# Optimization experiments

Hardware: AMD Instinct MI355X
Metric: run time of the kernel (lower is better)

## Reference

```python
import jax, jax.numpy as jnp
import numpy as np

NV, D, C, S, H, W = 50, 32, 16, 64, 64, 64  # views, volume res, feat ch, samples/ray, ray grid


def _conv(x, w, b, stride):
    y = jax.lax.conv_general_dilated(x, w, (stride, stride), 'SAME',
                                     dimension_numbers=('NCHW', 'OIHW', 'NCHW'))
    return y + b[None, :, None, None]


def setup_inputs():
    key = jax.random.key(0)
    k = jax.random.split(key, 16)
    images = jax.random.normal(k[0], (NV, 3, 128, 128), jnp.float32)
    # target_rays channels: [origin(3), dir(3), near(1), far(1)]
    o = (jax.random.uniform(k[1], (1, 3, H, W), jnp.float32) - 0.5) * 0.2
    d = jax.random.normal(k[2], (1, 3, H, W), jnp.float32)
    d = d / jnp.linalg.norm(d, axis=1, keepdims=True)
    near = jnp.full((1, 1, H, W), 0.2, jnp.float32)
    far = jnp.full((1, 1, H, W), 1.2, jnp.float32)
    target_rays = jnp.concatenate([o, d, near, far], axis=1)
    s = 0.1
    return {
        'images': images, 'target_rays': target_rays,
        'w1': jax.random.normal(k[3], (64, 3, 3, 3), jnp.float32) * s, 'b1': jnp.zeros((64,), jnp.float32),
        'w2': jax.random.normal(k[4], (128, 64, 3, 3), jnp.float32) * s, 'b2': jnp.zeros((128,), jnp.float32),
        'w3': jax.random.normal(k[5], (C * D, 128, 3, 3), jnp.float32) * s, 'b3': jnp.zeros((C * D,), jnp.float32),
        'mw1': jax.random.normal(k[6], (C, 64), jnp.float32) * s, 'mb1': jnp.zeros((64,), jnp.float32),
        'mw2': jax.random.normal(k[7], (64, 64), jnp.float32) * s, 'mb2': jnp.zeros((64,), jnp.float32),
        'mw3': jax.random.normal(k[8], (64, 4), jnp.float32) * s, 'mb3': jnp.zeros((4,), jnp.float32),
    }


def _forward(images, target_rays, w1, b1, w2, b2, w3, b3, mw1, mb1, mw2, mb2, mw3, mb3):
    # FeatureVolumeEncoder: [NV,3,128,128] -> per-view volume [NV,C,D,D,D]
    x = jax.nn.relu(_conv(images, w1, b1, 2))   # [NV,64,64,64]
    x = jax.nn.relu(_conv(x, w2, b2, 2))        # [NV,128,32,32]
    x = _conv(x, w3, b3, 1)                     # [NV,C*D,32,32]
    volumes = x.reshape(NV, C, D, D, D)
    # mean over views first: gather indices are identical per view, so
    # mean(gather(vol_i)) == gather(mean(vol_i)) by linearity (original means after sampling)
    vol = volumes.mean(axis=0)                  # [C,D,D,D]

    # sample_coarse_points: stratified z samples along each ray
    o, dirs = target_rays[0, 0:3], target_rays[0, 3:6]   # [3,H,W]
    near, far = target_rays[0, 6], target_rays[0, 7]     # [H,W]
    t = jnp.linspace(0.0, 1.0, S).astype(target_rays.dtype)[:, None, None]
    z = near[None] + (far - near)[None] * t              # [S,H,W]
    pts = o[:, None] + dirs[:, None] * z[None]           # [3,S,H,W]
    pts = pts.transpose(1, 2, 3, 0).reshape(-1, 3)       # [N,3], N=S*H*W

    # sample_from_3dgrid: trilinear interpolation, pts in [-1,1]^3
    c = jnp.clip((pts + 1.0) * 0.5 * (D - 1), 0.0, D - 1.0)
    c0 = jnp.minimum(jnp.floor(c).astype(jnp.int32), D - 2)
    f = c - c0
    ix, iy, iz = c0[:, 0], c0[:, 1], c0[:, 2]
    fx, fy, fz = f[:, 0], f[:, 1], f[:, 2]
    def g(dz, dy, dx):
        return vol[:, iz + dz, iy + dy, ix + dx]  # [C,N] irregular gather
    feat = (g(0, 0, 0) * (1 - fz) * (1 - fy) * (1 - fx) + g(0, 0, 1) * (1 - fz) * (1 - fy) * fx
          + g(0, 1, 0) * (1 - fz) * fy * (1 - fx) + g(0, 1, 1) * (1 - fz) * fy * fx
          + g(1, 0, 0) * fz * (1 - fy) * (1 - fx) + g(1, 0, 1) * fz * (1 - fy) * fx
          + g(1, 1, 0) * fz * fy * (1 - fx) + g(1, 1, 1) * fz * fy * fx)  # [C,N]
    feat = feat.T  # [N,C]

    # MLP_Nerf: 16 -> 64 -> 64 -> 4 (rgb, sigma)
    h = jax.nn.relu(feat @ mw1 + mb1)
    h = jax.nn.relu(h @ mw2 + mb2)
    raw = (h @ mw3 + mb3).reshape(S, H, W, 4)
    rgb = jax.nn.sigmoid(raw[..., :3])   # [S,H,W,3]
    sigma = jax.nn.relu(raw[..., 3])     # [S,H,W]

    # composite: quadrature alpha-compositing along samples
    deltas = jnp.concatenate([z[1:] - z[:-1], jnp.full((1, H, W), 1e10, z.dtype)], axis=0)
    alpha = 1.0 - jnp.exp(-sigma * deltas)
    trans = jnp.cumprod(1.0 - alpha + 1e-10, axis=0)
    trans = jnp.concatenate([jnp.ones((1, H, W), z.dtype), trans[:-1]], axis=0)
    wts = alpha * trans                  # [S,H,W]
    rgb_final = jnp.einsum('shw,shwc->chw', wts, rgb)[None, None]   # [1,1,3,H,W]
    depth_final = jnp.sum(wts * z, axis=0)[None, None, None]        # [1,1,1,H,W]
    return rgb_final, depth_final


def reference(images, target_rays, w1, b1, w2, b2, w3, b3, mw1, mb1, mw2, mb2, mw3, mb3):
    return _forward(images, target_rays, w1, b1, w2, b2, w3, b3, mw1, mb1, mw2, mb2, mw3, mb3)
```

## Files before the change

kernel.cpp:

```cpp
#include <hip/hip_runtime.h>
#include <hip/hip_bf16.h>

#define NVV 50
#define C1 64
#define C2 128
#define HW1 64
#define HW2 32

typedef short bf16x8 __attribute__((ext_vector_type(8)));
typedef short s16x4 __attribute__((ext_vector_type(4)));
typedef float f32x4 __attribute__((ext_vector_type(4)));
typedef int i32x4 __attribute__((ext_vector_type(4)));

__device__ inline short f2bf(float x) {
    unsigned u = __builtin_bit_cast(unsigned, x);
    unsigned r = (u + 0x7FFFu + ((u >> 16) & 1u)) >> 16;
    return (short)r;
}
__device__ inline float bf2f(short x) {
    unsigned u = ((unsigned)(unsigned short)x) << 16;
    return __builtin_bit_cast(float, u);
}

__global__ __launch_bounds__(256) void pack_all(const float* __restrict__ w1,
                                                const float* __restrict__ w2,
                                                const float* __restrict__ w3,
                                                const float* __restrict__ mw1, const float* __restrict__ mb1,
                                                const float* __restrict__ mw2, const float* __restrict__ mw3,
                                                __hip_bfloat16* __restrict__ WPK1,
                                                __hip_bfloat16* __restrict__ WPK2,
                                                __hip_bfloat16* __restrict__ WPK3,
                                                __hip_bfloat16* __restrict__ WPM1,
                                                __hip_bfloat16* __restrict__ WPM2,
                                                __hip_bfloat16* __restrict__ WPM3) {
    int i = blockIdx.x * 256 + threadIdx.x;
    if (i < 2048) {
        int j = i & 7, l = (i >> 3) & 63, mf = i >> 9;
        int oc = mf * 16 + (l & 15);
        int k = (l >> 4) * 8 + j;
        WPK1[i] = __float2bfloat16(k < 27 ? w1[oc * 27 + k] : 0.f);
    } else if (i < 75776) {
        int q = i - 2048;
        int j = q & 7, l = (q >> 3) & 63;
        int rest = q >> 9;
        int mtile = rest & 7;
        rest >>= 3;
        int icb = rest & 1;
        int kk = rest >> 1;
        int oc = mtile * 16 + (l & 15);
        int ic = icb * 32 + (l >> 4) * 8 + j;
        int ky = kk / 3, kx = kk % 3;
        WPK2[q] = __float2bfloat16(w2[((oc * 64 + ic) * 3 + ky) * 3 + kx]);
    } else if (i < 665600) {
        int q = i - 75776;
        int j = q & 7, l = (q >> 3) & 63;
        int rest = q >> 9;
        int m = rest & 31;
        rest >>= 5;
        int icb = rest & 3;
        int kk = rest >> 2;
        int oc = m * 16 + (l & 15);
        int ic = icb * 32 + (l >> 4) * 8 + j;
        int ky = kk / 3, kx = kk % 3;
        WPK3[q] = __float2bfloat16(w3[((oc * 128 + ic) * 3 + ky) * 3 + kx]);
    } else if (i < 672768) {
        int q = i - 665600;
        if (q < 2048) {
            int j = q & 7, l = (q >> 3) & 63, mf = q >> 9;
            int nn = mf * 16 + (l & 15);
            int ch = (l >> 4) * 8 + j;
            float v = ch < 16 ? mw1[ch * 64 + nn] : (ch == 16 ? mb1[nn] : 0.f);
            WPM1[q] = __float2bfloat16(v);
        } else if (q < 6144) {
            int p = q - 2048;
            int j = p & 7, l = (p >> 3) & 63, f = p >> 9;
            int kb = f >> 2, mf = f & 3;
            int nn = mf * 16 + (l & 15);
            int k = kb * 32 + (l >> 4) * 8 + j;
            WPM2[p] = __float2bfloat16(mw2[k * 64 + nn]);
        } else {
            int p = q - 6144;
            int j = p & 7, l = (p >> 3) & 63, kb = p >> 9;
            int m = l & 15;
            int k = kb * 32 + (l >> 4) * 8 + j;
            WPM3[p] = __float2bfloat16(m < 4 ? mw3[k * 4 + m] : 0.f);
        }
    }
}


__global__ __launch_bounds__(256) void conv1_fused(const float* __restrict__ img,
                                                   const __hip_bfloat16* __restrict__ wpack,
                                                   const float* __restrict__ b1,
                                                   __hip_bfloat16* __restrict__ out) {
    __shared__ float tile[3 * 9 * 132];
    int b = blockIdx.x;
    int xcd = b & 7, slot = b >> 3;
    int v = xcd + 8 * (slot >> 4);
    int oyb = slot & 15;
    if (v >= NVV) return;
    int tid = threadIdx.x;
    const float* ip = img + (size_t)v * 3 * 128 * 128;
    int iy0 = oyb * 8;
    for (int idx = tid; idx < 3456; idx += 256) {
        int ix = idx & 127;
        int t = idx >> 7;
        int iyl = t % 9, ic = t / 9;
        int iy = iy0 + iyl;
        tile[(ic * 9 + iyl) * 132 + ix] = (iy < 128) ? ip[(ic * 128 + iy) * 128 + ix] : 0.f;
    }
    if (tid < 108) {
        int c = tid & 3;
        int t = tid >> 2;
        int iyl = t % 9, ic = t / 9;
        tile[(ic * 9 + iyl) * 132 + 128 + c] = 0.f;
    }
    __syncthreads();

    int l = tid & 63, w = tid >> 6;
    int lane16 = l & 15, lgrp = l >> 4;
    int oy = oyb * 4 + w;

    int offj[8];
    bool okj[8];
    #pragma unroll
    for (int j = 0; j < 8; ++j) {
        int k = lgrp * 8 + j;
        bool ok = k < 27;
        int kc = ok ? k : 0;
        int ic = kc / 9, r = kc % 9;
        int ky = r / 3, kx = r % 3;
        offj[j] = (ic * 9 + 2 * w + ky) * 132 + kx;
        okj[j] = ok;
    }

    bf16x8 a[4];
    #pragma unroll
    for (int mf = 0; mf < 4; ++mf)
        a[mf] = *(const bf16x8*)((const short*)wpack + (mf * 64 + l) * 8);

    f32x4 acc[4][4];
    #pragma unroll
    for (int mf = 0; mf < 4; ++mf)
        #pragma unroll
        for (int nf = 0; nf < 4; ++nf)
            acc[mf][nf] = (f32x4){0.f, 0.f, 0.f, 0.f};

    #pragma unroll
    for (int nf = 0; nf < 4; ++nf) {
        int ox = nf * 16 + lane16;
        bf16x8 bb;
        #pragma unroll
        for (int j = 0; j < 8; ++j) {
            float x = tile[offj[j] + 2 * ox];
            bb[j] = okj[j] ? f2bf(x) : (short)0;
        }
        #pragma unroll
        for (int mf = 0; mf < 4; ++mf)
            acc[mf][nf] = __builtin_amdgcn_mfma_f32_16x16x32_bf16(a[mf], bb, acc[mf][nf], 0, 0, 0);
    }

    #pragma unroll
    for (int mf = 0; mf < 4; ++mf) {
        #pragma unroll
        for (int nf = 0; nf < 4; ++nf) {
            int px = (v * 64 + oy) * 64 + nf * 16 + lane16;
            s16x4 sv;
            #pragma unroll
            for (int r = 0; r < 4; ++r) {
                int oc = mf * 16 + lgrp * 4 + r;
                sv[r] = f2bf(fmaxf(acc[mf][nf][r] + b1[oc], 0.f));
            }
            *(s16x4*)((short*)out + (size_t)px * 64 + mf * 16 + lgrp * 4) = sv;
        }
    }
}

__global__ __launch_bounds__(128) void conv2_mfma(const __hip_bfloat16* __restrict__ A1c,
                                                  const __hip_bfloat16* __restrict__ wpack,
                                                  const float* __restrict__ b2,
                                                  __hip_bfloat16* __restrict__ A2c) {
    int b = blockIdx.x;
    int xcd = b & 7, slot = b >> 3;
    int v = xcd + 8 * (slot >> 4);
    int oyb = slot & 15;
    if (v >= NVV) return;
    int tid = threadIdx.x;
    int l = tid & 63;
    int wm = tid >> 6;
    int lane16 = l & 15, lgrp = l >> 4;

    int oxv[4], oyv[4];
    const short* pxb[4];
    bool rOOB[4], cOOB[4];
    const short* ibase = (const short*)A1c + (size_t)v * 64 * 64 * 64;
    #pragma unroll
    for (int nf = 0; nf < 4; ++nf) {
        int px = nf * 16 + lane16;
        int dy = px >> 5, ox = px & 31;
        oxv[nf] = ox;
        oyv[nf] = oyb * 2 + dy;
        pxb[nf] = ibase + ((size_t)(2 * oyv[nf]) * 64 + 2 * ox) * 64 + lgrp * 8;
        rOOB[nf] = (oyv[nf] == 31);
        cOOB[nf] = (ox == 31);
    }

    f32x4 acc[4][4];
    #pragma unroll
    for (int mf = 0; mf < 4; ++mf)
        #pragma unroll
        for (int nf = 0; nf < 4; ++nf)
            acc[mf][nf] = (f32x4){0.f, 0.f, 0.f, 0.f};

    const short* ab = (const short*)wpack + wm * 4 * 512 + l * 8;
    const bf16x8 bz = (bf16x8){0, 0, 0, 0, 0, 0, 0, 0};

    #pragma unroll
    for (int kk = 0; kk < 9; ++kk) {
        const int ky = kk / 3, kx = kk % 3;
        #pragma unroll
        for (int icb = 0; icb < 2; ++icb) {
            bf16x8 a[4];
            #pragma unroll
            for (int mf = 0; mf < 4; ++mf)
                a[mf] = *(const bf16x8*)(ab + ((kk * 2 + icb) * 8 + mf) * 512);

            bf16x8 bb[4];
            #pragma unroll
            for (int nf = 0; nf < 4; ++nf) {
                bf16x8 t = *(const bf16x8*)(pxb[nf] + (ky * 64 + kx) * 64 + icb * 32);
                bool dead = (ky == 2 && rOOB[nf]) || (kx == 2 && cOOB[nf]);
                bb[nf] = dead ? bz : t;
            }
            #pragma unroll
            for (int mf = 0; mf < 4; ++mf)
                #pragma unroll
                for (int nf = 0; nf < 4; ++nf)
                    acc[mf][nf] = __builtin_amdgcn_mfma_f32_16x16x32_bf16(a[mf], bb[nf], acc[mf][nf], 0, 0, 0);
        }
    }

    #pragma unroll
    for (int nf = 0; nf < 4; ++nf) {
        int pix = oyv[nf] * 32 + oxv[nf];
        short* ob = (short*)A2c + ((size_t)v * 1024 + pix) * 128 + wm * 64;
        #pragma unroll
        for (int mf = 0; mf < 4; ++mf) {
            f32x4 bv = *(const f32x4*)(b2 + wm * 64 + mf * 16 + lgrp * 4);
            s16x4 sv;
            #pragma unroll
            for (int r = 0; r < 4; ++r) sv[r] = f2bf(fmaxf(acc[mf][nf][r] + bv[r], 0.f));
            *(s16x4*)(ob + mf * 16 + lgrp * 4) = sv;
        }
    }
}

__global__ __launch_bounds__(256) void mean_kernel(const __hip_bfloat16* __restrict__ A2c,
                                                   __hip_bfloat16* __restrict__ XBc) {
    int i = blockIdx.x * 256 + threadIdx.x;
    int g = i & 15, pix = i >> 4;
    float acc[8] = {0.f, 0.f, 0.f, 0.f, 0.f, 0.f, 0.f, 0.f};
    for (int v = 0; v < NVV; ++v) {
        bf16x8 x = *(const bf16x8*)((const short*)A2c + ((size_t)v * 1024 + pix) * 128 + g * 8);
        #pragma unroll
        for (int j = 0; j < 8; ++j) acc[j] += bf2f(x[j]);
    }
    bf16x8 o;
    #pragma unroll
    for (int j = 0; j < 8; ++j) o[j] = f2bf(acc[j] * (1.0f / NVV));
    *(bf16x8*)((short*)XBc + (size_t)pix * 128 + g * 8) = o;
}

__global__ __launch_bounds__(128) void conv3_mfma(const __hip_bfloat16* __restrict__ XBc,
                                                  const __hip_bfloat16* __restrict__ wpack,
                                                  const float* __restrict__ b3,
                                                  __hip_bfloat16* __restrict__ VOLc) {
    int tid = threadIdx.x;
    int l = tid & 63;
    int wn = tid >> 6;
    int lane16 = l & 15, lgrp = l >> 4;

    int px = blockIdx.y * 32 + wn * 16 + lane16;
    int y = px >> 5, x = px & 31;

    const short* pxb = (const short*)XBc + ((ptrdiff_t)(y - 1) * 32 + (x - 1)) * 128 + lgrp * 8;
    bool tOOB = (y == 0), bOOB = (y == 31), lOOB = (x == 0), rOOB = (x == 31);

    f32x4 acc[4];
    #pragma unroll
    for (int mf = 0; mf < 4; ++mf) acc[mf] = (f32x4){0.f, 0.f, 0.f, 0.f};

    const short* ab = (const short*)wpack + (size_t)blockIdx.x * 4 * 512 + l * 8;
    const bf16x8 bzv = (bf16x8){0, 0, 0, 0, 0, 0, 0, 0};

    #pragma unroll
    for (int kk = 0; kk < 9; ++kk) {
        const int ky = kk / 3, kx = kk % 3;
        bool dead = (ky == 0 && tOOB) || (ky == 2 && bOOB) || (kx == 0 && lOOB) || (kx == 2 && rOOB);
        #pragma unroll
        for (int icb = 0; icb < 4; ++icb) {
            bf16x8 t = *(const bf16x8*)(pxb + (ky * 32 + kx) * 128 + icb * 32);
            bf16x8 bb = dead ? bzv : t;
            #pragma unroll
            for (int mf = 0; mf < 4; ++mf) {
                bf16x8 a = *(const bf16x8*)(ab + (size_t)((kk * 4 + icb) * 32 + mf) * 512);
                acc[mf] = __builtin_amdgcn_mfma_f32_16x16x32_bf16(a, bb, acc[mf], 0, 0, 0);
            }
        }
    }

    int oc_base = blockIdx.x * 64;
    #pragma unroll
    for (int mf = 0; mf < 4; ++mf) {
        f32x4 bv = *(const f32x4*)(b3 + oc_base + mf * 16 + lgrp * 4);
        #pragma unroll
        for (int r = 0; r < 4; ++r) {
            int oc = oc_base + mf * 16 + lgrp * 4 + r;
            int c = oc >> 5, iz = oc & 31;
            VOLc[((size_t)((iz * 32 + y) * 32 + x)) * 16 + c] = __float2bfloat16(acc[mf][r] + bv[r]);
        }
    }
}

__global__ __launch_bounds__(256) void mlp_render(const __hip_bfloat16* __restrict__ VOLc,
                                                  const float* __restrict__ rays,
                                                  const __hip_bfloat16* __restrict__ wpm1,
                                                  const __hip_bfloat16* __restrict__ wpm2,
                                                  const __hip_bfloat16* __restrict__ wpm3,
                                                  const float* __restrict__ mb2,
                                                  const float* __restrict__ mb3,
                                                  float* __restrict__ out) {
    __shared__ short hbuf[4][32 * 72];
    __shared__ f32x4 rawb[4][64];
    int tid = threadIdx.x;
    int w = tid >> 6, l = tid & 63;
    int lane16 = l & 15, lgrp = l >> 4;
    short* hb = hbuf[w];
    int pix = blockIdx.x * 4 + w;

    bf16x8 a1[4];
    #pragma unroll
    for (int mf = 0; mf < 4; ++mf)
        a1[mf] = *(const bf16x8*)((const short*)wpm1 + (mf * 64 + l) * 8);
    bf16x8 a2[2][4];
    #pragma unroll
    for (int kb = 0; kb < 2; ++kb)
        #pragma unroll
        for (int mf = 0; mf < 4; ++mf)
            a2[kb][mf] = *(const bf16x8*)((const short*)wpm2 + ((kb * 4 + mf) * 64 + l) * 8);
    bf16x8 a3[2];
    a3[0] = *(const bf16x8*)((const short*)wpm3 + (0 * 64 + l) * 8);
    a3[1] = *(const bf16x8*)((const short*)wpm3 + (1 * 64 + l) * 8);
    f32x4 b3v = *(const f32x4*)(mb3);

    const bf16x8 bz = (bf16x8){0, 0, 0, 0, 0, 0, 0, 0};
    const bf16x8 bbias = (bf16x8){(short)0x3F80, 0, 0, 0, 0, 0, 0, 0};

    float o0 = rays[pix], o1 = rays[4096 + pix], o2 = rays[2 * 4096 + pix];
    float d0 = rays[3 * 4096 + pix], d1 = rays[4 * 4096 + pix], d2 = rays[5 * 4096 + pix];
    float nearv = rays[6 * 4096 + pix], farv = rays[7 * 4096 + pix];

    int nfg = l >> 5, hf = (l >> 4) & 1;

    for (int rep = 0; rep < 2; ++rep) {
        int s = rep * 32 + nfg * 16 + lane16;
        float t = (float)s / 63.0f;
        float z = nearv + (farv - nearv) * t;
        float px = o0 + d0 * z, py = o1 + d1 * z, pz = o2 + d2 * z;
        float cx = fminf(fmaxf((px + 1.f) * 15.5f, 0.f), 31.f);
        float cy = fminf(fmaxf((py + 1.f) * 15.5f, 0.f), 31.f);
        float cz = fminf(fmaxf((pz + 1.f) * 15.5f, 0.f), 31.f);
        int ix = min((int)floorf(cx), 30);
        int iy = min((int)floorf(cy), 30);
        int iz = min((int)floorf(cz), 30);
        float fx = cx - (float)ix, fy = cy - (float)iy, fz = cz - (float)iz;
        float gx = 1.f - fx, gy = 1.f - fy, gz = 1.f - fz;
        float wv[8] = {gz * gy * gx, gz * gy * fx, gz * fy * gx, gz * fy * fx,
                       fz * gy * gx, fz * gy * fx, fz * fy * gx, fz * fy * fx};
        const int co[8] = {0, 16, 512, 528, 16384, 16400, 16896, 16912};
        int base = (iz * 32 + iy) * 32 + ix;
        const short* vp = (const short*)VOLc + (size_t)base * 16 + hf * 8;

        float f8[8] = {0.f, 0.f, 0.f, 0.f, 0.f, 0.f, 0.f, 0.f};
        #pragma unroll
        for (int c = 0; c < 8; ++c) {
            bf16x8 cv = *(const bf16x8*)(vp + co[c]);
            #pragma unroll
            for (int j = 0; j < 8; ++j) f8[j] += wv[c] * bf2f(cv[j]);
        }
        bf16x8 own;
        #pragma unroll
        for (int j = 0; j < 8; ++j) own[j] = f2bf(f8[j]);

        i32x4 oi = __builtin_bit_cast(i32x4, own);
        i32x4 si;
        si[0] = __shfl_xor(oi[0], 32);
        si[1] = __shfl_xor(oi[1], 32);
        si[2] = __shfl_xor(oi[2], 32);
        si[3] = __shfl_xor(oi[3], 32);
        bf16x8 swf = __builtin_bit_cast(bf16x8, si);

        bf16x8 b0 = (lgrp < 2) ? own : ((lgrp == 2) ? bbias : bz);
        bf16x8 b1 = (lgrp < 2) ? swf : ((lgrp == 2) ? bbias : bz);

        f32x4 acc1[4][2];
        #pragma unroll
        for (int mf = 0; mf < 4; ++mf) {
            acc1[mf][0] = (f32x4){0.f, 0.f, 0.f, 0.f};
            acc1[mf][1] = (f32x4){0.f, 0.f, 0.f, 0.f};
            acc1[mf][0] = __builtin_amdgcn_mfma_f32_16x16x32_bf16(a1[mf], b0, acc1[mf][0], 0, 0, 0);
            acc1[mf][1] = __builtin_amdgcn_mfma_f32_16x16x32_bf16(a1[mf], b1, acc1[mf][1], 0, 0, 0);
        }
        #pragma unroll
        for (int mf = 0; mf < 4; ++mf) {
            #pragma unroll
            for (int nf = 0; nf < 2; ++nf) {
                s16x4 sv;
                #pragma unroll
                for (int r = 0; r < 4; ++r) sv[r] = f2bf(fmaxf(acc1[mf][nf][r], 0.f));
                *(s16x4*)(hb + (nf * 16 + lane16) * 72 + mf * 16 + lgrp * 4) = sv;
            }
        }

        f32x4 acc2[4][2];
        #pragma unroll
        for (int mf = 0; mf < 4; ++mf) {
            acc2[mf][0] = (f32x4){0.f, 0.f, 0.f, 0.f};
            acc2[mf][1] = (f32x4){0.f, 0.f, 0.f, 0.f};
        }
        #pragma unroll
        for (int nf = 0; nf < 2; ++nf) {
            #pragma unroll
            for (int kb = 0; kb < 2; ++kb) {
                bf16x8 bh = *(const bf16x8*)(hb + (nf * 16 + lane16) * 72 + kb * 32 + lgrp * 8);
                #pragma unroll
                for (int mf = 0; mf < 4; ++mf)
                    acc2[mf][nf] = __builtin_amdgcn_mfma_f32_16x16x32_bf16(a2[kb][mf], bh, acc2[mf][nf], 0, 0, 0);
            }
        }
        #pragma unroll
        for (int mf = 0; mf < 4; ++mf) {
            f32x4 bv = *(const f32x4*)(mb2 + mf * 16 + lgrp * 4);
            #pragma unroll
            for (int nf = 0; nf < 2; ++nf) {
                s16x4 sv;
                #pragma unroll
                for (int r = 0; r < 4; ++r) sv[r] = f2bf(fmaxf(acc2[mf][nf][r] + bv[r], 0.f));
                *(s16x4*)(hb + (nf * 16 + lane16) * 72 + mf * 16 + lgrp * 4) = sv;
            }
        }

        f32x4 acc3[2];
        acc3[0] = (f32x4){0.f, 0.f, 0.f, 0.f};
        acc3[1] = (f32x4){0.f, 0.f, 0.f, 0.f};
        #pragma unroll
        for (int nf = 0; nf < 2; ++nf) {
            #pragma unroll
            for (int kb = 0; kb < 2; ++kb) {
                bf16x8 bh = *(const bf16x8*)(hb + (nf * 16 + lane16) * 72 + kb * 32 + lgrp * 8);
                acc3[nf] = __builtin_amdgcn_mfma_f32_16x16x32_bf16(a3[kb], bh, acc3[nf], 0, 0, 0);
            }
        }
        if (lgrp == 0) {
            #pragma unroll
            for (int nf = 0; nf < 2; ++nf)
                rawb[w][rep * 32 + nf * 16 + lane16] = acc3[nf] + b3v;
        }
    }

    f32x4 rv = rawb[w][l];
    float dz = (farv - nearv) * (1.f / 63.f);
    float zl = nearv + (farv - nearv) * ((float)l / 63.0f);
    float delta = (l == 63) ? 1e10f : dz;
    float sigma = fmaxf(rv[3], 0.f);
    float alpha = 1.f - __expf(-sigma * delta);
    float la = __builtin_log2f(1.f - alpha + 1e-10f);

    float inc = la;
    #pragma unroll
    for (int off = 1; off < 64; off <<= 1) {
        float y = __shfl_up(inc, off);
        if (l >= off) inc += y;
    }
    float T = __builtin_exp2f(inc - la);
    float wt = alpha * T;

    float cr = wt / (1.f + __expf(-rv[0]));
    float cg = wt / (1.f + __expf(-rv[1]));
    float cb = wt / (1.f + __expf(-rv[2]));
    float cd = wt * zl;

    #pragma unroll
    for (int off = 32; off > 0; off >>= 1) {
        cr += __shfl_down(cr, off);
        cg += __shfl_down(cg, off);
        cb += __shfl_down(cb, off);
        cd += __shfl_down(cd, off);
    }
    if (l == 0) {
        out[pix]             = cr;
        out[4096 + pix]      = cg;
        out[2 * 4096 + pix]  = cb;
        out[12288 + pix]     = cd;
    }
}

extern "C" void kernel_launch(void* const* d_in, const int* in_sizes, int n_in,
                              void* d_out, int out_size, void* d_ws, size_t ws_size,
                              hipStream_t stream) {
    const float* images = (const float*)d_in[0];
    const float* rays   = (const float*)d_in[1];
    const float* w1 = (const float*)d_in[2];
    const float* b1 = (const float*)d_in[3];
    const float* w2 = (const float*)d_in[4];
    const float* b2 = (const float*)d_in[5];
    const float* w3 = (const float*)d_in[6];
    const float* b3 = (const float*)d_in[7];
    const float* mw1 = (const float*)d_in[8];
    const float* mb1 = (const float*)d_in[9];
    const float* mw2 = (const float*)d_in[10];
    const float* mb2 = (const float*)d_in[11];
    const float* mw3 = (const float*)d_in[12];
    const float* mb3 = (const float*)d_in[13];
    float* out = (float*)d_out;

    __hip_bfloat16* A1c  = (__hip_bfloat16*)d_ws;
    __hip_bfloat16* WPK2 = A1c + 13107200;
    __hip_bfloat16* WPK1 = WPK2 + 73728;
    __hip_bfloat16* VOLc = WPK1 + 2048;
    __hip_bfloat16* WPM1 = VOLc + 524288;
    __hip_bfloat16* WPM2 = WPM1 + 2048;
    __hip_bfloat16* WPM3 = WPM2 + 4096;
    __hip_bfloat16* A2c  = WPM3 + 1024;
    __hip_bfloat16* XBc  = A2c + 6553600;
    __hip_bfloat16* WPK3 = XBc + 131072;

    pack_all<<<dim3(2628), dim3(256), 0, stream>>>(w1, w2, w3, mw1, mb1, mw2, mw3,
                                                   WPK1, WPK2, WPK3, WPM1, WPM2, WPM3);
    conv1_fused<<<dim3(896), dim3(256), 0, stream>>>(images, WPK1, b1, A1c);
    conv2_mfma<<<dim3(896), dim3(128), 0, stream>>>(A1c, WPK2, b2, A2c);
    mean_kernel<<<dim3(64), dim3(256), 0, stream>>>(A2c, XBc);
    conv3_mfma<<<dim3(8, 32), dim3(128), 0, stream>>>(XBc, WPK3, b3, VOLc);
    mlp_render<<<dim3(1024), dim3(256), 0, stream>>>(VOLc, rays, WPM1, WPM2, WPM3, mb2, mb3, out);
}
```

Baseline: 86.78 us.

## Merge weight packing into conv1 and fold view-mean into conv2 via last-block counter

Weight packing now runs in extra blocks of the conv1 launch, and conv1 builds its own bf16 A fragments from w1 staged in shared memory instead of reading a pre-packed buffer. The separate mean kernel is removed: each conv2 block bumps a per-row atomic counter, and the last block to finish a row computes the mean over all views for that row. This cuts two kernel launches and the gaps between them. In exchange the mean for a row is done by a single block that runs serially at the tail, and correctness now depends on threadfence ordering and on the counters being reset every call.

```diff
diff --git a/kernel.cpp b/kernel.cpp
--- a/kernel.cpp
+++ b/kernel.cpp
@@ -22,84 +22,83 @@
     return __builtin_bit_cast(float, u);
 }
 
-__global__ __launch_bounds__(256) void pack_all(const float* __restrict__ w1,
-                                                const float* __restrict__ w2,
-                                                const float* __restrict__ w3,
-                                                const float* __restrict__ mw1, const float* __restrict__ mb1,
-                                                const float* __restrict__ mw2, const float* __restrict__ mw3,
-                                                __hip_bfloat16* __restrict__ WPK1,
-                                                __hip_bfloat16* __restrict__ WPK2,
-                                                __hip_bfloat16* __restrict__ WPK3,
-                                                __hip_bfloat16* __restrict__ WPM1,
-                                                __hip_bfloat16* __restrict__ WPM2,
-                                                __hip_bfloat16* __restrict__ WPM3) {
-    int i = blockIdx.x * 256 + threadIdx.x;
-    if (i < 2048) {
-        int j = i & 7, l = (i >> 3) & 63, mf = i >> 9;
-        int oc = mf * 16 + (l & 15);
-        int k = (l >> 4) * 8 + j;
-        WPK1[i] = __float2bfloat16(k < 27 ? w1[oc * 27 + k] : 0.f);
-    } else if (i < 75776) {
-        int q = i - 2048;
-        int j = q & 7, l = (q >> 3) & 63;
-        int rest = q >> 9;
-        int mtile = rest & 7;
-        rest >>= 3;
-        int icb = rest & 1;
-        int kk = rest >> 1;
-        int oc = mtile * 16 + (l & 15);
-        int ic = icb * 32 + (l >> 4) * 8 + j;
-        int ky = kk / 3, kx = kk % 3;
-        WPK2[q] = __float2bfloat16(w2[((oc * 64 + ic) * 3 + ky) * 3 + kx]);
-    } else if (i < 665600) {
-        int q = i - 75776;
-        int j = q & 7, l = (q >> 3) & 63;
-        int rest = q >> 9;
-        int m = rest & 31;
-        rest >>= 5;
-        int icb = rest & 3;
-        int kk = rest >> 2;
-        int oc = m * 16 + (l & 15);
-        int ic = icb * 32 + (l >> 4) * 8 + j;
-        int ky = kk / 3, kx = kk % 3;
-        WPK3[q] = __float2bfloat16(w3[((oc * 128 + ic) * 3 + ky) * 3 + kx]);
-    } else if (i < 672768) {
-        int q = i - 665600;
-        if (q < 2048) {
-            int j = q & 7, l = (q >> 3) & 63, mf = q >> 9;
-            int nn = mf * 16 + (l & 15);
-            int ch = (l >> 4) * 8 + j;
-            float v = ch < 16 ? mw1[ch * 64 + nn] : (ch == 16 ? mb1[nn] : 0.f);
-            WPM1[q] = __float2bfloat16(v);
-        } else if (q < 6144) {
-            int p = q - 2048;
-            int j = p & 7, l = (p >> 3) & 63, f = p >> 9;
-            int kb = f >> 2, mf = f & 3;
-            int nn = mf * 16 + (l & 15);
-            int k = kb * 32 + (l >> 4) * 8 + j;
-            WPM2[p] = __float2bfloat16(mw2[k * 64 + nn]);
-        } else {
-            int p = q - 6144;
-            int j = p & 7, l = (p >> 3) & 63, kb = p >> 9;
-            int m = l & 15;
-            int k = kb * 32 + (l >> 4) * 8 + j;
-            WPM3[p] = __float2bfloat16(m < 4 ? mw3[k * 4 + m] : 0.f);
-        }
-    }
-}
-
-
-__global__ __launch_bounds__(256) void conv1_fused(const float* __restrict__ img,
-                                                   const __hip_bfloat16* __restrict__ wpack,
-                                                   const float* __restrict__ b1,
-                                                   __hip_bfloat16* __restrict__ out) {
+__global__ __launch_bounds__(256) void conv1_pack(const float* __restrict__ img,
+                                                  const float* __restrict__ w1,
+                                                  const float* __restrict__ b1,
+                                                  const float* __restrict__ w2,
+                                                  const float* __restrict__ w3,
+                                                  const float* __restrict__ mw1, const float* __restrict__ mb1,
+                                                  const float* __restrict__ mw2, const float* __restrict__ mw3,
+                                                  __hip_bfloat16* __restrict__ A1c,
+                                                  __hip_bfloat16* __restrict__ WPK2,
+                                                  __hip_bfloat16* __restrict__ WPK3,
+                                                  __hip_bfloat16* __restrict__ WPM1,
+                                                  __hip_bfloat16* __restrict__ WPM2,
+                                                  __hip_bfloat16* __restrict__ WPM3,
+                                                  int* __restrict__ CNT) {
     __shared__ float tile[3 * 9 * 132];
+    __shared__ float w1s[1728];
     int b = blockIdx.x;
+    int tid = threadIdx.x;
+
+    if (b >= 896) {
+        int i = (b - 896) * 256 + tid;
+        if (i < 16) CNT[i] = 0;
+        if (i < 2048) {
+        } else if (i < 75776) {
+            int q = i - 2048;
+            int j = q & 7, l = (q >> 3) & 63;
+            int rest = q >> 9;
+            int mtile = rest & 7;
+            rest >>= 3;
+            int icb = rest & 1;
+            int kk = rest >> 1;
+            int oc = mtile * 16 + (l & 15);
+            int ic = icb * 32 + (l >> 4) * 8 + j;
+            int ky = kk / 3, kx = kk % 3;
+            WPK2[q] = __float2bfloat16(w2[((oc * 64 + ic) * 3 + ky) * 3 + kx]);
+        } else if (i < 665600) {
+            int q = i - 75776;
+            int j = q & 7, l = (q >> 3) & 63;
+            int rest = q >> 9;
+            int m = rest & 31;
+            rest >>= 5;
+            int icb = rest & 3;
+            int kk = rest >> 2;
+            int oc = m * 16 + (l & 15);
+            int ic = icb * 32 + (l >> 4) * 8 + j;
+            int ky = kk / 3, kx = kk % 3;
+            WPK3[q] = __float2bfloat16(w3[((oc * 128 + ic) * 3 + ky) * 3 + kx]);
+        } else if (i < 672768) {
+            int q = i - 665600;
+            if (q < 2048) {
+                int j = q & 7, l = (q >> 3) & 63, mf = q >> 9;
+                int nn = mf * 16 + (l & 15);
+                int ch = (l >> 4) * 8 + j;
+                float v = ch < 16 ? mw1[ch * 64 + nn] : (ch == 16 ? mb1[nn] : 0.f);
+                WPM1[q] = __float2bfloat16(v);
+            } else if (q < 6144) {
+                int p = q - 2048;
+                int j = p & 7, l = (p >> 3) & 63, f = p >> 9;
+                int kb = f >> 2, mf = f & 3;
+                int nn = mf * 16 + (l & 15);
+                int k = kb * 32 + (l >> 4) * 8 + j;
+                WPM2[p] = __float2bfloat16(mw2[k * 64 + nn]);
+            } else {
+                int p = q - 6144;
+                int j = p & 7, l = (p >> 3) & 63, kb = p >> 9;
+                int m = l & 15;
+                int k = kb * 32 + (l >> 4) * 8 + j;
+                WPM3[p] = __float2bfloat16(m < 4 ? mw3[k * 4 + m] : 0.f);
+            }
+        }
+        return;
+    }
+
     int xcd = b & 7, slot = b >> 3;
     int v = xcd + 8 * (slot >> 4);
     int oyb = slot & 15;
     if (v >= NVV) return;
-    int tid = threadIdx.x;
     const float* ip = img + (size_t)v * 3 * 128 * 128;
     int iy0 = oyb * 8;
     for (int idx = tid; idx < 3456; idx += 256) {
@@ -115,6 +114,7 @@
         int iyl = t % 9, ic = t / 9;
         tile[(ic * 9 + iyl) * 132 + 128 + c] = 0.f;
     }
+    for (int i = tid; i < 1728; i += 256) w1s[i] = w1[i];
     __syncthreads();
 
     int l = tid & 63, w = tid >> 6;
@@ -136,8 +136,13 @@
 
     bf16x8 a[4];
     #pragma unroll
-    for (int mf = 0; mf < 4; ++mf)
-        a[mf] = *(const bf16x8*)((const short*)wpack + (mf * 64 + l) * 8);
+    for (int mf = 0; mf < 4; ++mf) {
+        #pragma unroll
+        for (int j = 0; j < 8; ++j) {
+            int k = lgrp * 8 + j;
+            a[mf][j] = (k < 27) ? f2bf(w1s[(mf * 16 + lane16) * 27 + k]) : (short)0;
+        }
+    }
 
     f32x4 acc[4][4];
     #pragma unroll
@@ -171,15 +176,18 @@
                 int oc = mf * 16 + lgrp * 4 + r;
                 sv[r] = f2bf(fmaxf(acc[mf][nf][r] + b1[oc], 0.f));
             }
-            *(s16x4*)((short*)out + (size_t)px * 64 + mf * 16 + lgrp * 4) = sv;
-        }
-    }
-}
-
-__global__ __launch_bounds__(128) void conv2_mfma(const __hip_bfloat16* __restrict__ A1c,
+            *(s16x4*)((short*)A1c + (size_t)px * 64 + mf * 16 + lgrp * 4) = sv;
+        }
+    }
+}
+
+__global__ __launch_bounds__(128) void conv2_mean(const __hip_bfloat16* __restrict__ A1c,
                                                   const __hip_bfloat16* __restrict__ wpack,
                                                   const float* __restrict__ b2,
-                                                  __hip_bfloat16* __restrict__ A2c) {
+                                                  __hip_bfloat16* __restrict__ A2c,
+                                                  __hip_bfloat16* __restrict__ XBc,
+                                                  int* __restrict__ CNT) {
+    __shared__ int isLast;
     int b = blockIdx.x;
     int xcd = b & 7, slot = b >> 3;
     int v = xcd + 8 * (slot >> 4);
@@ -253,22 +261,30 @@
             *(s16x4*)(ob + mf * 16 + lgrp * 4) = sv;
         }
     }
-}
-
-__global__ __launch_bounds__(256) void mean_kernel(const __hip_bfloat16* __restrict__ A2c,
-                                                   __hip_bfloat16* __restrict__ XBc) {
-    int i = blockIdx.x * 256 + threadIdx.x;
-    int g = i & 15, pix = i >> 4;
-    float acc[8] = {0.f, 0.f, 0.f, 0.f, 0.f, 0.f, 0.f, 0.f};
-    for (int v = 0; v < NVV; ++v) {
-        bf16x8 x = *(const bf16x8*)((const short*)A2c + ((size_t)v * 1024 + pix) * 128 + g * 8);
-        #pragma unroll
-        for (int j = 0; j < 8; ++j) acc[j] += bf2f(x[j]);
-    }
-    bf16x8 o;
-    #pragma unroll
-    for (int j = 0; j < 8; ++j) o[j] = f2bf(acc[j] * (1.0f / NVV));
-    *(bf16x8*)((short*)XBc + (size_t)pix * 128 + g * 8) = o;
+
+    __threadfence();
+    if (tid == 0) {
+        int old = atomicAdd(&CNT[oyb], 1);
+        isLast = (old == NVV - 1) ? 1 : 0;
+    }
+    __syncthreads();
+    if (isLast) {
+        __threadfence();
+        for (int it = tid; it < 1024; it += 128) {
+            int pp = oyb * 64 + (it >> 4);
+            int g = it & 15;
+            float accm[8] = {0.f, 0.f, 0.f, 0.f, 0.f, 0.f, 0.f, 0.f};
+            for (int vv = 0; vv < NVV; ++vv) {
+                bf16x8 x = *(const bf16x8*)((const short*)A2c + ((size_t)vv * 1024 + pp) * 128 + g * 8);
+                #pragma unroll
+                for (int j = 0; j < 8; ++j) accm[j] += bf2f(x[j]);
+            }
+            bf16x8 o;
+            #pragma unroll
+            for (int j = 0; j < 8; ++j) o[j] = f2bf(accm[j] * (1.0f / NVV));
+            *(bf16x8*)((short*)XBc + (size_t)pp * 128 + g * 8) = o;
+        }
+    }
 }
 
 __global__ __launch_bounds__(128) void conv3_mfma(const __hip_bfloat16* __restrict__ XBc,
@@ -534,12 +550,11 @@
     __hip_bfloat16* A2c  = WPM3 + 1024;
     __hip_bfloat16* XBc  = A2c + 6553600;
     __hip_bfloat16* WPK3 = XBc + 131072;
-
-    pack_all<<<dim3(2628), dim3(256), 0, stream>>>(w1, w2, w3, mw1, mb1, mw2, mw3,
-                                                   WPK1, WPK2, WPK3, WPM1, WPM2, WPM3);
-    conv1_fused<<<dim3(896), dim3(256), 0, stream>>>(images, WPK1, b1, A1c);
-    conv2_mfma<<<dim3(896), dim3(128), 0, stream>>>(A1c, WPK2, b2, A2c);
-    mean_kernel<<<dim3(64), dim3(256), 0, stream>>>(A2c, XBc);
+    int* CNT             = (int*)(WPK3 + 589824);
+
+    conv1_pack<<<dim3(3524), dim3(256), 0, stream>>>(images, w1, b1, w2, w3, mw1, mb1, mw2, mw3,
+                                                     A1c, WPK2, WPK3, WPM1, WPM2, WPM3, CNT);
+    conv2_mean<<<dim3(896), dim3(128), 0, stream>>>(A1c, WPK2, b2, A2c, XBc, CNT);
     conv3_mfma<<<dim3(8, 32), dim3(128), 0, stream>>>(XBc, WPK3, b3, VOLc);
     mlp_render<<<dim3(1024), dim3(256), 0, stream>>>(VOLc, rays, WPM1, WPM2, WPM3, mb2, mb3, out);
 }
```

Measured after the change: 173.2 us. +99.6%, slower.
